# Kernel tuning notes

Hardware: AMD Instinct MI355X
Metric: run time of the kernel (lower is better)

Reference implementation:

```python
import jax, jax.numpy as jnp
import numpy as np

EPS = 1e-05


def setup_inputs() -> dict:
    key = jax.random.key(0)
    k1, k2, k3, k4 = jax.random.split(key, 4)
    B, N, L, J = 1, 256, 192, 32
    n_feat_out = 128
    d2 = J * J  # 1024
    x_down = jax.random.normal(k1, (B, N, L, J), dtype=jnp.float32)
    x_down_w = jax.random.normal(k2, (B, N, L, J), dtype=jnp.float32)
    a_2 = jnp.ones((d2,), dtype=jnp.float32)
    b_2 = jnp.zeros((d2,), dtype=jnp.float32)
    # nn.Linear default init: U(-1/sqrt(fan_in), 1/sqrt(fan_in))
    bound = 1.0 / np.sqrt(d2)
    W = jax.random.uniform(k3, (d2, n_feat_out), dtype=jnp.float32, minval=-bound, maxval=bound)
    b = jax.random.uniform(k4, (n_feat_out,), dtype=jnp.float32, minval=-bound, maxval=bound)
    return {"x_down": x_down, "x_down_w": x_down_w, "a_2": a_2, "b_2": b_2, "W": W, "b": b}


def reference(x_down, x_down_w, a_2, b_2, W, b):
    B, N, L, J = x_down.shape
    # outer-product contraction over MSA dim: (B,L,L,J,J)
    pair = jnp.einsum('bnij,bnlm->biljm', x_down, x_down_w)
    pair = pair.reshape(B, L, L, J * J)
    # LayerNorm over last dim (biased variance, matching torch unbiased=False)
    mean = pair.mean(axis=-1, keepdims=True)
    var = pair.var(axis=-1, keepdims=True)
    pair = a_2 * (pair - mean) / jnp.sqrt(var + EPS) + b_2
    # Linear projection J^2 -> n_feat_out
    return pair @ W + b
```

## Files before the change

### kernel.cpp

```cpp
#include <hip/hip_runtime.h>
#include <hip/hip_bf16.h>
#include <stdint.h>

#define NN   256
#define LL   192
#define MDIM 6144
#define D2   1024
#define FF   128

typedef __bf16 bf16x8 __attribute__((ext_vector_type(8)));
typedef float  f32x4  __attribute__((ext_vector_type(4)));

#define MFMA16(a, b, c) __builtin_amdgcn_mfma_f32_16x16x32_bf16(a, b, c, 0, 0, 0)

__device__ __forceinline__ void gload_lds16(const void* g, void* l) {
  __builtin_amdgcn_global_load_lds(
      (__attribute__((address_space(1))) void*)(g),
      (__attribute__((address_space(3))) void*)(l),
      16, 0, 0);
}

static __device__ __forceinline__ unsigned short bf16_bits(float v) {
  __bf16 h = (__bf16)v;
  return __builtin_bit_cast(unsigned short, h);
}

__global__ __launch_bounds__(256)
void prep_all(const float* __restrict__ x1, const float* __restrict__ x2,
              const float* __restrict__ W, const float* __restrict__ a2,
              const float* __restrict__ b2, const float* __restrict__ bias,
              __bf16* __restrict__ At, __bf16* __restrict__ Bt,
              __bf16* __restrict__ WB, float* __restrict__ S,
              float* __restrict__ T) {
  __shared__ float tile[32][33];
  const int b = blockIdx.x;
  const int t = threadIdx.x;
  if (b < 3072) {
    const float* src = (b < 1536) ? x1 : x2;
    __bf16* dst = (b < 1536) ? At : Bt;
    const int bb = (b < 1536) ? b : b - 1536;
    const int m0 = (bb % 192) * 32;
    const int k0 = (bb / 192) * 32;
    {
      const int kr = t >> 3, mc = (t & 7) * 4;
      const float4 v = *(const float4*)&src[(size_t)(k0 + kr) * MDIM + m0 + mc];
      tile[kr][mc + 0] = v.x;
      tile[kr][mc + 1] = v.y;
      tile[kr][mc + 2] = v.z;
      tile[kr][mc + 3] = v.w;
    }
    __syncthreads();
    {
      const int mr = t >> 3, kc = (t & 7) * 4;
      ushort4 u;
      u.x = bf16_bits(tile[kc + 0][mr]);
      u.y = bf16_bits(tile[kc + 1][mr]);
      u.z = bf16_bits(tile[kc + 2][mr]);
      u.w = bf16_bits(tile[kc + 3][mr]);
      *(ushort4*)&dst[(size_t)(m0 + mr) * NN + k0 + kc] = u;
    }
  } else {
    const int f = b - 3072;
    float s = 0.f, tt = 0.f;
#pragma unroll
    for (int it = 0; it < 4; ++it) {
      const int k = t + it * 256;
      const float wv = W[(size_t)k * FF + f];
      const __bf16 wa = (__bf16)(a2[k] * wv);
      WB[(size_t)(k >> 5) * 4096 + f * 32 + ((k >> 3) & 3) * 8 + (k & 7)] = wa;
      s += (float)wa;
      tt += b2[k] * wv;
    }
#pragma unroll
    for (int off = 32; off; off >>= 1) {
      s += __shfl_xor(s, off);
      tt += __shfl_xor(tt, off);
    }
    const int wv_ = t >> 6, ln = t & 63;
    if (ln == 0) { tile[0][wv_] = s; tile[1][wv_] = tt; }
    __syncthreads();
    if (t == 0) {
      S[f] = tile[0][0] + tile[0][1] + tile[0][2] + tile[0][3];
      T[f] = tile[1][0] + tile[1][1] + tile[1][2] + tile[1][3] + bias[f];
    }
  }
}

__global__ __launch_bounds__(256, 4)
void fused8(const __bf16* __restrict__ At, const __bf16* __restrict__ Bt,
            const __bf16* __restrict__ WB, const float* __restrict__ S,
            const float* __restrict__ T, float* __restrict__ out) {
  __shared__ uint8_t lds[32768];
  __shared__ float mean_s[16], rstd_s[16];

  const int tid = threadIdx.x;
  const int w = tid >> 6;
  const int lane = tid & 63;
  const int q = lane >> 4;
  const int c = lane & 15;

  const int b = blockIdx.x;
  const int xcd = b & 7;
  const int s_ = b >> 3;
  const int bx = (xcd >> 1) * 12 + (s_ % 12);
  const int by = (xcd & 1) * 24 + (s_ / 12);
  const int m0 = bx * 128, n0 = by * 128;

  uint8_t* As = lds;
  uint8_t* Bs = lds + 16384;

  const int l8 = lane & 7;
  const int r8 = lane >> 3;
  const int gsw = l8 ^ r8;

  f32x4 acc[4][4];
#pragma unroll
  for (int i = 0; i < 4; ++i)
#pragma unroll
    for (int j = 0; j < 4; ++j)
      acc[i][j] = (f32x4){0.f, 0.f, 0.f, 0.f};

  const int mbase = (w & 1) * 64;
  const int nbase = (w >> 1) * 64;

  {
    const __bf16* gA = At + (size_t)(m0 + w * 8 + r8) * NN + gsw * 8;
    const __bf16* gB = Bt + (size_t)(n0 + w * 8 + r8) * NN + gsw * 8;
    uint8_t* dst = As + (w * 8) * 128;
#pragma unroll 1
    for (int kb = 0; kb < 4; ++kb) {
      __syncthreads();
#pragma unroll
      for (int s4 = 0; s4 < 4; ++s4) {
        gload_lds16(gA + (size_t)s4 * 32 * NN, dst + s4 * 4096);
        gload_lds16(gB + (size_t)s4 * 32 * NN, dst + 16384 + s4 * 4096);
      }
      __syncthreads();
#pragma unroll
      for (int ks = 0; ks < 2; ++ks) {
        const int slot = ((ks * 4 + q) ^ (lane & 7)) * 16;
        bf16x8 a[4];
#pragma unroll
        for (int t4 = 0; t4 < 4; ++t4)
          a[t4] = *(const bf16x8*)(As + (mbase + t4 * 16 + c) * 128 + slot);
#pragma unroll
        for (int tj = 0; tj < 4; ++tj) {
          const bf16x8 bfr =
              *(const bf16x8*)(Bs + (nbase + tj * 16 + c) * 128 + slot);
#pragma unroll
          for (int ti = 0; ti < 4; ++ti)
            acc[ti][tj] = MFMA16(a[ti], bfr, acc[ti][tj]);
        }
      }
      gA += 64;
      gB += 64;
    }
  }

  const int fb = w * 32;
  const __bf16* wb0 = WB + (fb + c) * 32 + q * 8;
  const __bf16* wb1 = WB + (fb + 16 + c) * 32 + q * 8;
  bf16x8 pb0[8], pb1[8];
  pb0[0] = *(const bf16x8*)(wb0);
  pb0[1] = *(const bf16x8*)(wb0 + 4096);
  pb1[0] = *(const bf16x8*)(wb1);
  pb1[1] = *(const bf16x8*)(wb1 + 4096);

  __syncthreads();

  const int i_hi = w & 1, l_hi = w >> 1;
#pragma unroll
  for (int ab = 0; ab < 2; ++ab) {
#pragma unroll
    for (int cb = 0; cb < 2; ++cb) {
      float s1 = 0.f, s2 = 0.f;
#pragma unroll
      for (int dti = 0; dti < 2; ++dti)
#pragma unroll
        for (int dtj = 0; dtj < 2; ++dtj)
#pragma unroll
          for (int reg = 0; reg < 4; ++reg) {
            const float v = acc[ab * 2 + dti][cb * 2 + dtj][reg];
            s1 += v; s2 += v * v;
          }
#pragma unroll
      for (int off = 32; off; off >>= 1) {
        s1 += __shfl_xor(s1, off);
        s2 += __shfl_xor(s2, off);
      }
      const float mean = s1 * (1.0f / 1024.0f);
      const float var = s2 * (1.0f / 1024.0f) - mean * mean;
      const float rstd = rsqrtf(var + 1e-5f);
      const int r = (i_hi * 2 + ab) * 4 + (l_hi * 2 + cb);
      if (lane == 0) { mean_s[r] = mean; rstd_s[r] = rstd; }
      const int r7 = r & 7;
#pragma unroll
      for (int dti = 0; dti < 2; ++dti)
#pragma unroll
        for (int dtj = 0; dtj < 2; ++dtj)
#pragma unroll
          for (int rp = 0; rp < 4; rp += 2) {
            const float x = acc[ab * 2 + dti][cb * 2 + dtj][rp];
            const float y = acc[ab * 2 + dti][cb * 2 + dtj][rp + 1];
            const float send = (c & 1) ? x : y;
            const float recv = __shfl_xor(send, 1);
            const float vlo = (c & 1) ? recv : x;
            const float vhi = (c & 1) ? y : recv;
            const int reg_w = (c & 1) ? rp + 1 : rp;
            const int j = dti * 16 + q * 4 + reg_w;
            const int mm0 = dtj * 16 + (c & ~1);
            const int k = j * 32 + mm0;
            const int g = k >> 3;
            const int G = g ^ (g >> 4) ^ r7;
            const uint32_t dw =
                ((uint32_t)bf16_bits(vhi) << 16) | (uint32_t)bf16_bits(vlo);
            *(uint32_t*)(lds + r * 2048 + G * 16 + (mm0 & 7) * 2) = dw;
          }
    }
  }

  __syncthreads();
  __builtin_amdgcn_sched_barrier(0);

#pragma unroll
  for (int p = 2; p < 8; ++p) {
    pb0[p] = *(const bf16x8*)(wb0 + p * 4096);
    pb1[p] = *(const bf16x8*)(wb1 + p * 4096);
  }

  f32x4 acc2[2];
  acc2[0] = (f32x4){0.f, 0.f, 0.f, 0.f};
  acc2[1] = (f32x4){0.f, 0.f, 0.f, 0.f};
  const int c7 = c & 7;
#pragma unroll
  for (int kstep = 0; kstep < 32; ++kstep) {
    const int g = kstep * 4 + q;
    const int G = g ^ (g >> 4) ^ c7;
    const bf16x8 av = *(const bf16x8*)(lds + c * 2048 + G * 16);
    acc2[0] = MFMA16(av, pb0[kstep & 7], acc2[0]);
    acc2[1] = MFMA16(av, pb1[kstep & 7], acc2[1]);
    if (kstep < 24) {
      pb0[kstep & 7] = *(const bf16x8*)(wb0 + (kstep + 8) * 4096);
      pb1[kstep & 7] = *(const bf16x8*)(wb1 + (kstep + 8) * 4096);
    }
  }

  const float S0 = S[fb + c], T0 = T[fb + c];
  const float S1 = S[fb + 16 + c], T1 = T[fb + 16 + c];
#pragma unroll
  for (int reg = 0; reg < 4; ++reg) {
    const int r = q * 4 + reg;
    const float mean = mean_s[r], rstd = rstd_s[r];
    const int i = bx * 4 + (r >> 2);
    const int l = by * 4 + (r & 3);
    const size_t base = ((size_t)i * LL + l) * FF;
    out[base + fb + c]      = rstd * (acc2[0][reg] - mean * S0) + T0;
    out[base + fb + 16 + c] = rstd * (acc2[1][reg] - mean * S1) + T1;
  }
}

extern "C" void kernel_launch(void* const* d_in, const int* in_sizes, int n_in,
                              void* d_out, int out_size, void* d_ws, size_t ws_size,
                              hipStream_t stream) {
  const float* x_down   = (const float*)d_in[0];
  const float* x_down_w = (const float*)d_in[1];
  const float* a2       = (const float*)d_in[2];
  const float* b2       = (const float*)d_in[3];
  const float* W        = (const float*)d_in[4];
  const float* bias     = (const float*)d_in[5];
  float* out = (float*)d_out;

  uint8_t* ws = (uint8_t*)d_ws;
  __bf16* At  = (__bf16*)(ws);
  __bf16* Bt  = (__bf16*)(ws + 3145728);
  __bf16* WB  = (__bf16*)(ws + 6291456);
  float*  S   = (float*)(ws + 6553600);
  float*  T   = (float*)(ws + 6554112);

  prep_all<<<dim3(3200), dim3(256), 0, stream>>>(x_down, x_down_w, W, a2, b2,
                                                 bias, At, Bt, WB, S, T);
  fused8<<<dim3(2304), dim3(256), 0, stream>>>(At, Bt, WB, S, T, out);
}
```

Measured before the change: 131.3 us.

## Load GEMM operand fragments directly from global memory, bypassing LDS staging

The main GEMM loop stops staging A and B tiles through LDS with global_load_lds and block barriers. Each wave now reads its MFMA fragments straight from global memory (in practice from L2/L1) in 16-byte loads, one k-slice of 32 per iteration. This drops the LDS round-trip and the __syncthreads pairs. In exchange, the two waves that share a 64-row slice each load it separately, doubling global traffic and exposing load latency with no software prefetch.

```diff
diff --git a/kernel.cpp b/kernel.cpp
--- a/kernel.cpp
+++ b/kernel.cpp
@@ -12,13 +12,6 @@
 typedef float  f32x4  __attribute__((ext_vector_type(4)));
 
 #define MFMA16(a, b, c) __builtin_amdgcn_mfma_f32_16x16x32_bf16(a, b, c, 0, 0, 0)
-
-__device__ __forceinline__ void gload_lds16(const void* g, void* l) {
-  __builtin_amdgcn_global_load_lds(
-      (__attribute__((address_space(1))) void*)(g),
-      (__attribute__((address_space(3))) void*)(l),
-      16, 0, 0);
-}
 
 static __device__ __forceinline__ unsigned short bf16_bits(float v) {
   __bf16 h = (__bf16)v;
@@ -87,7 +80,7 @@
 }
 
 __global__ __launch_bounds__(256, 4)
-void fused8(const __bf16* __restrict__ At, const __bf16* __restrict__ Bt,
+void fused9(const __bf16* __restrict__ At, const __bf16* __restrict__ Bt,
             const __bf16* __restrict__ WB, const float* __restrict__ S,
             const float* __restrict__ T, float* __restrict__ out) {
   __shared__ uint8_t lds[32768];
@@ -106,12 +99,8 @@
   const int by = (xcd & 1) * 24 + (s_ / 12);
   const int m0 = bx * 128, n0 = by * 128;
 
-  uint8_t* As = lds;
-  uint8_t* Bs = lds + 16384;
-
-  const int l8 = lane & 7;
-  const int r8 = lane >> 3;
-  const int gsw = l8 ^ r8;
+  const int mbase = (w & 1) * 64;
+  const int nbase = (w >> 1) * 64;
 
   f32x4 acc[4][4];
 #pragma unroll
@@ -120,40 +109,24 @@
     for (int j = 0; j < 4; ++j)
       acc[i][j] = (f32x4){0.f, 0.f, 0.f, 0.f};
 
-  const int mbase = (w & 1) * 64;
-  const int nbase = (w >> 1) * 64;
-
   {
-    const __bf16* gA = At + (size_t)(m0 + w * 8 + r8) * NN + gsw * 8;
-    const __bf16* gB = Bt + (size_t)(n0 + w * 8 + r8) * NN + gsw * 8;
-    uint8_t* dst = As + (w * 8) * 128;
+    const __bf16* pa = At + (size_t)(m0 + mbase + c) * NN + q * 8;
+    const __bf16* pb = Bt + (size_t)(n0 + nbase + c) * NN + q * 8;
 #pragma unroll 1
-    for (int kb = 0; kb < 4; ++kb) {
-      __syncthreads();
-#pragma unroll
-      for (int s4 = 0; s4 < 4; ++s4) {
-        gload_lds16(gA + (size_t)s4 * 32 * NN, dst + s4 * 4096);
-        gload_lds16(gB + (size_t)s4 * 32 * NN, dst + 16384 + s4 * 4096);
+    for (int ks = 0; ks < 8; ++ks) {
+      bf16x8 a[4], bfr[4];
+#pragma unroll
+      for (int t4 = 0; t4 < 4; ++t4) {
+        a[t4]   = *(const bf16x8*)(pa + (size_t)t4 * 16 * NN);
+        bfr[t4] = *(const bf16x8*)(pb + (size_t)t4 * 16 * NN);
       }
-      __syncthreads();
-#pragma unroll
-      for (int ks = 0; ks < 2; ++ks) {
-        const int slot = ((ks * 4 + q) ^ (lane & 7)) * 16;
-        bf16x8 a[4];
-#pragma unroll
-        for (int t4 = 0; t4 < 4; ++t4)
-          a[t4] = *(const bf16x8*)(As + (mbase + t4 * 16 + c) * 128 + slot);
-#pragma unroll
-        for (int tj = 0; tj < 4; ++tj) {
-          const bf16x8 bfr =
-              *(const bf16x8*)(Bs + (nbase + tj * 16 + c) * 128 + slot);
-#pragma unroll
-          for (int ti = 0; ti < 4; ++ti)
-            acc[ti][tj] = MFMA16(a[ti], bfr, acc[ti][tj]);
-        }
-      }
-      gA += 64;
-      gB += 64;
+#pragma unroll
+      for (int ti = 0; ti < 4; ++ti)
+#pragma unroll
+        for (int tj = 0; tj < 4; ++tj)
+          acc[ti][tj] = MFMA16(a[ti], bfr[tj], acc[ti][tj]);
+      pa += 32;
+      pb += 32;
     }
   }
 
@@ -165,8 +138,6 @@
   pb0[1] = *(const bf16x8*)(wb0 + 4096);
   pb1[0] = *(const bf16x8*)(wb1);
   pb1[1] = *(const bf16x8*)(wb1 + 4096);
-
-  __syncthreads();
 
   const int i_hi = w & 1, l_hi = w >> 1;
 #pragma unroll
@@ -279,5 +250,5 @@
 
   prep_all<<<dim3(3200), dim3(256), 0, stream>>>(x_down, x_down_w, W, a2, b2,
                                                  bias, At, Bt, WB, S, T);
-  fused8<<<dim3(2304), dim3(256), 0, stream>>>(At, Bt, WB, S, T, out);
-}
+  fused9<<<dim3(2304), dim3(256), 0, stream>>>(At, Bt, WB, S, T, out);
+}
```

After: 180.8 us. +37.7%, slower.
